# Kernel optimization log

Hardware: AMD Instinct MI355X
Metric: run time of the kernel (lower is better)

## Reference

```python
import jax, jax.numpy as jnp
import numpy as np

B, N, D, C, S = 128, 100000, 256, 2000, 751  # batch, memory size, feat dim, num classes, source classes
TEMP = 0.05
EPS = 1e-06


def _l2norm(x):
    return x / jnp.linalg.norm(x, axis=-1, keepdims=True)


def setup_inputs() -> dict:
    key = jax.random.key(0)
    k1, k2, k3, k4, k5 = jax.random.split(key, 5)
    inputs = _l2norm(jax.random.normal(k1, (B, D), dtype=jnp.float32))
    inputs2 = _l2norm(jax.random.normal(k2, (B, D), dtype=jnp.float32))
    features = _l2norm(jax.random.normal(k3, (N, D), dtype=jnp.float32))
    labels = jax.random.randint(k4, (N,), 0, C)
    labels = labels.at[:C].set(jnp.arange(C))  # ensure labels.max()+1 == C
    indexes = jax.random.randint(k5, (B,), 0, N)
    return {"inputs": inputs, "inputs2": inputs2, "features": features,
            "labels": labels, "indexes": indexes, "source_classes": S}


def reference(inputs, inputs2, features, labels, indexes, source_classes):
    # memory-bank logits, [B, N]
    logits = (inputs @ features.T) / TEMP
    logits2 = (inputs2 @ features.T) / TEMP
    targets = labels[indexes]  # [B]

    # per-class counts and segment-mean of logits over the bank, [C, B]
    nums = jax.ops.segment_sum(jnp.ones((N,), jnp.float32), labels, num_segments=C)  # [C]
    denom = jnp.where(nums > 0, nums, 1.0)[:, None]  # [C, 1]
    sim = jax.ops.segment_sum(logits.T, labels, num_segments=C) / denom   # [C, B]
    sim2 = jax.ops.segment_sum(logits2.T, labels, num_segments=C) / denom  # [C, B]

    # MSE between class-probability maps over the first source_classes classes
    p1 = sim[:source_classes].T   # [B, S]
    p2 = sim2[:source_classes].T  # [B, S]
    diff = jax.nn.softmax(p1, axis=1) - jax.nn.softmax(p2, axis=1)
    loss_mse = jnp.sum(diff * diff) / source_classes

    # hard-positive/negative mining: per-class max of logits (0 for empty classes)
    seg_max = jax.ops.segment_max(logits.T, labels, num_segments=C)  # [C, B], -inf where empty
    present = (nums > 0)  # [C]
    sim_hard = jnp.where(present[:, None], seg_max, 0.0).T  # [B, C]
    # for the target class, use the hardest (min) positive instead
    seg_min = jax.ops.segment_min(logits.T, labels, num_segments=C)  # [C, B]
    b_idx = jnp.arange(B)
    sim_hard = sim_hard.at[b_idx, targets].set(seg_min[targets, b_idx])

    # masked softmax over present classes + NLL
    mask = present.astype(jnp.float32)[None, :]  # [1, C]
    exps = jnp.exp(sim_hard) * mask
    masked_sim = exps / (jnp.sum(exps, axis=1, keepdims=True) + EPS)
    loss_con = -jnp.mean(jnp.log(masked_sim[b_idx, targets] + EPS))

    return (loss_con, loss_mse)
```

## Files before the change

kernel.cpp:

```cpp
#include <hip/hip_runtime.h>
#include <hip/hip_bf16.h>

#define BB 128
#define NN 100000
#define DD 256
#define CC 2000
#define SS 751
#define INVTEMP 20.0f
#define EPSV 1e-6f

#define HIST_BLOCKS 391
#define PREP_BLOCKS 32
#define COPY_BLOCKS 3125
#define NTILES_MAX 3563

typedef __attribute__((ext_vector_type(8))) short bf16x8;
typedef __attribute__((ext_vector_type(8))) unsigned short u16x8;
typedef __attribute__((ext_vector_type(4))) float f32x4;

__device__ __forceinline__ unsigned short f2bf(float x) {
    unsigned int u = __float_as_uint(x);
    u += 0x7fffu + ((u >> 16) & 1u);
    return (unsigned short)(u >> 16);
}

__device__ __forceinline__ u16x8 pack8(float4 a, float4 b) {
    u16x8 o;
    o[0] = f2bf(a.x); o[1] = f2bf(a.y); o[2] = f2bf(a.z); o[3] = f2bf(a.w);
    o[4] = f2bf(b.x); o[5] = f2bf(b.y); o[6] = f2bf(b.z); o[7] = f2bf(b.w);
    return o;
}

__global__ __launch_bounds__(256) void hist_prep_kernel(
    const int* __restrict__ labels, int* __restrict__ counts,
    const float* __restrict__ in1, const float* __restrict__ in2,
    unsigned short* __restrict__ inb)
{
    int bid = blockIdx.x;
    if (bid < HIST_BLOCKS) {
        int n = bid * 256 + threadIdx.x;
        if (n < NN) atomicAdd(&counts[labels[n]], 1);
    } else {
        int ch = (bid - HIST_BLOCKS) * 256 + threadIdx.x;
        if (ch >= 8192) return;
        int l  = ch & 63;
        int kc = (ch >> 6) & 7;
        int nr = ch >> 9;
        int row = nr * 16 + (l & 15);
        const float* src = (row < BB) ? (in1 + (size_t)row * DD)
                                      : (in2 + (size_t)(row - BB) * DD);
        int k0 = kc * 32 + ((l >> 4) << 3);
        u16x8 o;
        #pragma unroll
        for (int j = 0; j < 8; ++j) o[j] = f2bf(src[k0 + j]);
        *(u16x8*)(inb + (size_t)ch * 8) = o;
    }
}

__global__ __launch_bounds__(256) void scan_kernel(const int* __restrict__ counts,
                                                   int* __restrict__ tile_start,
                                                   int* __restrict__ cursor,
                                                   int* __restrict__ tile_meta,
                                                   int* __restrict__ ntiles_total,
                                                   float* __restrict__ out) {
    const int PT = 8;
    int tid = threadIdx.x;
    if (tid == 0) { out[0] = 0.f; out[1] = 0.f; }
    int tcnt[PT];
    int tot = 0;
    #pragma unroll
    for (int i = 0; i < PT; ++i) {
        int c = tid * PT + i;
        tcnt[i] = (c < CC) ? ((counts[c] + 63) >> 6) : 0;
        tot += tcnt[i];
    }
    __shared__ int sh[256];
    sh[tid] = tot;
    __syncthreads();
    for (int ofs = 1; ofs < 256; ofs <<= 1) {
        int v = (tid >= ofs) ? sh[tid - ofs] : 0;
        __syncthreads();
        sh[tid] += v;
        __syncthreads();
    }
    if (tid == 255) *ntiles_total = sh[255];
    int run = sh[tid] - tot;
    #pragma unroll
    for (int i = 0; i < PT; ++i) {
        int c = tid * PT + i;
        if (c < CC) {
            tile_start[c] = run;
            cursor[c] = run << 6;
            for (int j = 0; j < tcnt[i]; ++j)
                tile_meta[run + j] = (c << 5) | j;
        }
        run += tcnt[i];
    }
}

__global__ __launch_bounds__(256) void scatter_conv(
    const int* __restrict__ labels, int* __restrict__ cursor,
    const float* __restrict__ features, unsigned short* __restrict__ featbf)
{
    int t = blockIdx.x * 256 + threadIdx.x;
    int n = t >> 3;
    int g = t & 7;
    int c = labels[n];
    int p = 0;
    if (g == 0) p = atomicAdd(&cursor[c], 1);
    p = __shfl(p, (threadIdx.x & 63) & ~7, 64);

    const float4* src = (const float4*)(features + (size_t)n * DD) + g * 8;
    unsigned short* dst = featbf + (size_t)p * 256 + g * 32;
    #pragma unroll
    for (int i = 0; i < 4; ++i) {
        float4 a = src[2 * i], b = src[2 * i + 1];
        *(u16x8*)(dst + i * 8) = pack8(a, b);
    }
}

__global__ __launch_bounds__(512, 4) void mm_kernel(
    const unsigned short* __restrict__ featbf, const unsigned short* __restrict__ inb,
    const int* __restrict__ tile_meta, const int* __restrict__ counts,
    const int* __restrict__ ntiles_total,
    float* __restrict__ part_max, float* __restrict__ part_min,
    float* __restrict__ part_sA, float* __restrict__ part_sB)
{
    const int t = blockIdx.x;
    if (t >= *ntiles_total) return;
    const int tid = threadIdx.x;
    const int w   = tid >> 6;
    const int l   = tid & 63;
    const int meta = tile_meta[t];
    const int c    = meta >> 5;
    const int base_local = (meta & 31) << 6;
    const int cnt  = counts[c];

    __shared__ __align__(16) char ldsA[32768];

    bf16x8 bfr[16];
    #pragma unroll
    for (int kc = 0; kc < 8; ++kc)
        #pragma unroll
        for (int nb = 0; nb < 2; ++nb) {
            int nr = 2 * w + nb;
            bfr[kc * 2 + nb] = *(const bf16x8*)(inb + (((size_t)(nr * 8 + kc) * 64 + l) << 3));
        }

    const char* Abase = (const char*)featbf + ((size_t)t << 15);
    #pragma unroll
    for (int i = 0; i < 4; ++i) {
        int f   = w * 4 + i;
        int kc  = f & 7;
        int row = ((f >> 3) << 4) + ((l & 15) ^ kc);
        const char* src = Abase + (row << 9) + (kc << 6) + ((l >> 4) << 4);
        __builtin_amdgcn_global_load_lds(
            (const __attribute__((address_space(1))) void*)src,
            (__attribute__((address_space(3))) void*)(&ldsA[0] + (f << 10)),
            16, 0, 0);
    }
    __syncthreads();

    f32x4 acc[4][2];
    #pragma unroll
    for (int ma = 0; ma < 4; ++ma)
        #pragma unroll
        for (int nb = 0; nb < 2; ++nb)
            acc[ma][nb] = (f32x4){0.f, 0.f, 0.f, 0.f};

    __builtin_amdgcn_s_setprio(1);
    #pragma unroll
    for (int kc = 0; kc < 8; ++kc) {
        int lx = (l ^ kc) << 4;
        #pragma unroll
        for (int ma = 0; ma < 4; ++ma) {
            bf16x8 a = *(const bf16x8*)(&ldsA[0] + ((ma * 8 + kc) << 10) + lx);
            acc[ma][0] = __builtin_amdgcn_mfma_f32_16x16x32_bf16(a, bfr[kc * 2 + 0], acc[ma][0], 0, 0, 0);
            acc[ma][1] = __builtin_amdgcn_mfma_f32_16x16x32_bf16(a, bfr[kc * 2 + 1], acc[ma][1], 0, 0, 0);
        }
    }
    __builtin_amdgcn_s_setprio(0);

    const int h4 = (l >> 4) << 2;
    float sm[2] = {0.f, 0.f};
    float mx[2] = {-3.4e38f, -3.4e38f};
    float mn[2] = { 3.4e38f,  3.4e38f};
    #pragma unroll
    for (int ma = 0; ma < 4; ++ma) {
        #pragma unroll
        for (int reg = 0; reg < 4; ++reg) {
            bool valid = (base_local + 16 * ma + h4 + reg) < cnt;
            if (valid) {
                #pragma unroll
                for (int nb = 0; nb < 2; ++nb) {
                    float v = acc[ma][nb][reg];
                    sm[nb] += v;
                    if (w < 4) {
                        mx[nb] = fmaxf(mx[nb], v);
                        mn[nb] = fminf(mn[nb], v);
                    }
                }
            }
        }
    }
    #pragma unroll
    for (int nb = 0; nb < 2; ++nb) {
        sm[nb] += __shfl_xor(sm[nb], 16);
        sm[nb] += __shfl_xor(sm[nb], 32);
        if (w < 4) {
            mx[nb] = fmaxf(mx[nb], __shfl_xor(mx[nb], 16));
            mx[nb] = fmaxf(mx[nb], __shfl_xor(mx[nb], 32));
            mn[nb] = fminf(mn[nb], __shfl_xor(mn[nb], 16));
            mn[nb] = fminf(mn[nb], __shfl_xor(mn[nb], 32));
        }
    }
    if (l < 16) {
        #pragma unroll
        for (int nb = 0; nb < 2; ++nb) {
            int col = 32 * (w & 3) + 16 * nb + l;
            size_t p = (size_t)t * 128 + col;
            if (w < 4) { part_max[p] = mx[nb]; part_min[p] = mn[nb]; part_sA[p] = sm[nb]; }
            else       { part_sB[p] = sm[nb]; }
        }
    }
}

__global__ __launch_bounds__(128) void combine_kernel(
    const float* __restrict__ part_max, const float* __restrict__ part_min,
    const float* __restrict__ part_sA, const float* __restrict__ part_sB,
    const int* __restrict__ tile_start, const int* __restrict__ counts,
    float* __restrict__ gmax, float* __restrict__ gmin,
    float* __restrict__ simA, float* __restrict__ simB)
{
    const int c   = blockIdx.x;
    const int col = threadIdx.x;
    const int cnt = counts[c];
    const size_t o = (size_t)c * 128 + col;
    if (cnt <= 0) {
        gmax[o] = 0.f; gmin[o] = 0.f; simA[o] = 0.f; simB[o] = 0.f;
        return;
    }
    const int t0 = tile_start[c];
    const int nt = (cnt + 63) >> 6;
    float mx = -3.4e38f, mn = 3.4e38f, sA = 0.f, sB = 0.f;
    for (int j = 0; j < nt; ++j) {
        size_t p = (size_t)(t0 + j) * 128 + col;
        mx = fmaxf(mx, part_max[p]);
        mn = fminf(mn, part_min[p]);
        sA += part_sA[p];
        sB += part_sB[p];
    }
    float icnt = INVTEMP / (float)cnt;
    gmax[o] = mx * INVTEMP;
    gmin[o] = mn * INVTEMP;
    simA[o] = sA * icnt;
    simB[o] = sB * icnt;
}


__device__ __forceinline__ float blk_reduce_sum(float v) {
    __shared__ float sh[4];
    int lane = threadIdx.x & 63, w = threadIdx.x >> 6;
    #pragma unroll
    for (int o = 32; o; o >>= 1) v += __shfl_down(v, o, 64);
    __syncthreads();
    if (lane == 0) sh[w] = v;
    __syncthreads();
    return sh[0] + sh[1] + sh[2] + sh[3];
}

__device__ __forceinline__ float blk_reduce_max(float v) {
    __shared__ float sh[4];
    int lane = threadIdx.x & 63, w = threadIdx.x >> 6;
    #pragma unroll
    for (int o = 32; o; o >>= 1) v = fmaxf(v, __shfl_down(v, o, 64));
    __syncthreads();
    if (lane == 0) sh[w] = v;
    __syncthreads();
    return fmaxf(fmaxf(sh[0], sh[1]), fmaxf(sh[2], sh[3]));
}

__global__ __launch_bounds__(256) void finalize_kernel(
    const float* __restrict__ gmax, const float* __restrict__ gmin,
    const float* __restrict__ simA, const float* __restrict__ simB,
    const int* __restrict__ counts, const int* __restrict__ labels,
    const int* __restrict__ indexes, float* __restrict__ out)
{
    const int b   = blockIdx.x;
    const int tid = threadIdx.x;
    const int tgt = labels[indexes[b]];

    __shared__ float sh_etgt;
    float local = 0.f;
    for (int c = tid; c < CC; c += 256) {
        float e = 0.f;
        if (counts[c] > 0) {
            float v = (c == tgt) ? gmin[(size_t)c * 128 + b] : gmax[(size_t)c * 128 + b];
            e = expf(v);
        }
        local += e;
        if (c == tgt) sh_etgt = e;
    }
    float sum_e = blk_reduce_sum(local);
    float etgt = sh_etgt;
    float loss_con_b = -logf(etgt / (sum_e + EPSV) + EPSV);

    __shared__ float a1[SS], a2[SS];
    for (int c = tid; c < SS; c += 256) {
        a1[c] = simA[(size_t)c * 128 + b];
        a2[c] = simB[(size_t)c * 128 + b];
    }
    __syncthreads();
    float m1 = -3.4e38f, m2 = -3.4e38f;
    for (int c = tid; c < SS; c += 256) { m1 = fmaxf(m1, a1[c]); m2 = fmaxf(m2, a2[c]); }
    m1 = blk_reduce_max(m1);
    m2 = blk_reduce_max(m2);
    float s1 = 0.f, s2 = 0.f;
    for (int c = tid; c < SS; c += 256) { s1 += expf(a1[c] - m1); s2 += expf(a2[c] - m2); }
    s1 = blk_reduce_sum(s1);
    s2 = blk_reduce_sum(s2);
    float inv1 = 1.f / s1, inv2 = 1.f / s2;
    float dsum = 0.f;
    for (int c = tid; c < SS; c += 256) {
        float d = expf(a1[c] - m1) * inv1 - expf(a2[c] - m2) * inv2;
        dsum += d * d;
    }
    dsum = blk_reduce_sum(dsum);
    if (tid == 0) {
        atomicAdd(&out[0], loss_con_b * (1.0f / (float)BB));
        atomicAdd(&out[1], dsum * (1.0f / (float)SS));
    }
}


extern "C" void kernel_launch(void* const* d_in, const int* in_sizes, int n_in,
                              void* d_out, int out_size, void* d_ws, size_t ws_size,
                              hipStream_t stream) {
    const float* inputs   = (const float*)d_in[0];
    const float* inputs2  = (const float*)d_in[1];
    const float* features = (const float*)d_in[2];
    const int*   labels   = (const int*)d_in[3];
    const int*   indexes  = (const int*)d_in[4];

    float* out = (float*)d_out;

    int* wsi = (int*)d_ws;
    int* counts     = wsi;
    int* tile_start = wsi + 2048;
    int* cursor     = wsi + 4096;
    int* ntiles     = wsi + 6144;
    unsigned short* inb = (unsigned short*)(wsi + 6160);
    int* tile_meta  = wsi + 38928;
    float* part_max = (float*)(wsi + 42496);
    float* part_min = part_max + (size_t)NTILES_MAX * 128;
    float* part_sA  = part_min + (size_t)NTILES_MAX * 128;
    float* part_sB  = part_sA  + (size_t)NTILES_MAX * 128;
    float* gmax = part_sB + (size_t)NTILES_MAX * 128;
    float* gmin = gmax + (size_t)CC * 128;
    float* simA = gmin + (size_t)CC * 128;
    float* simB = simA + (size_t)CC * 128;
    unsigned short* featbf = (unsigned short*)(simB + (size_t)CC * 128);

    hipMemsetAsync(counts, 0, 2048 * sizeof(int), stream);

    hist_prep_kernel<<<HIST_BLOCKS + PREP_BLOCKS, 256, 0, stream>>>(
        labels, counts, inputs, inputs2, inb);
    scan_kernel<<<1, 256, 0, stream>>>(counts, tile_start, cursor, tile_meta, ntiles, out);
    scatter_conv<<<COPY_BLOCKS, 256, 0, stream>>>(labels, cursor, features, featbf);
    mm_kernel<<<NTILES_MAX, 512, 0, stream>>>(featbf, inb, tile_meta, counts, ntiles,
                                              part_max, part_min, part_sA, part_sB);
    combine_kernel<<<CC, 128, 0, stream>>>(part_max, part_min, part_sA, part_sB,
                                           tile_start, counts, gmax, gmin, simA, simB);
    finalize_kernel<<<BB, 256, 0, stream>>>(gmax, gmin, simA, simB, counts,
                                            labels, indexes, out);
}
```

Before: 103.4 us.

## Process two tiles per matmul block and fold combine into finalize

The matmul kernel now loads two feature tiles into a doubled LDS buffer per block, reusing the register-resident input fragments across both tiles and halving the block count. The separate per-class combine kernel is removed, and finalize reads tile partials directly, computing class max/min/mean per batch column. This saves one launch and the intermediate global arrays. In exchange, LDS use per block doubles, which may reduce occupancy, and finalize does strided partial reads with only 128 blocks.

```diff
diff --git a/kernel.cpp b/kernel.cpp
--- a/kernel.cpp
+++ b/kernel.cpp
@@ -13,6 +13,7 @@
 #define PREP_BLOCKS 32
 #define COPY_BLOCKS 3125
 #define NTILES_MAX 3563
+#define NBLK2 1782
 
 typedef __attribute__((ext_vector_type(8))) short bf16x8;
 typedef __attribute__((ext_vector_type(8))) unsigned short u16x8;
@@ -126,17 +127,14 @@
     float* __restrict__ part_max, float* __restrict__ part_min,
     float* __restrict__ part_sA, float* __restrict__ part_sB)
 {
-    const int t = blockIdx.x;
-    if (t >= *ntiles_total) return;
+    const int ntt = *ntiles_total;
+    const int t0g = 2 * blockIdx.x;
+    if (t0g >= ntt) return;
     const int tid = threadIdx.x;
     const int w   = tid >> 6;
     const int l   = tid & 63;
-    const int meta = tile_meta[t];
-    const int c    = meta >> 5;
-    const int base_local = (meta & 31) << 6;
-    const int cnt  = counts[c];
-
-    __shared__ __align__(16) char ldsA[32768];
+
+    __shared__ __align__(16) char ldsA[2][32768];
 
     bf16x8 bfr[16];
     #pragma unroll
@@ -147,170 +145,170 @@
             bfr[kc * 2 + nb] = *(const bf16x8*)(inb + (((size_t)(nr * 8 + kc) * 64 + l) << 3));
         }
 
-    const char* Abase = (const char*)featbf + ((size_t)t << 15);
-    #pragma unroll
-    for (int i = 0; i < 4; ++i) {
-        int f   = w * 4 + i;
-        int kc  = f & 7;
-        int row = ((f >> 3) << 4) + ((l & 15) ^ kc);
-        const char* src = Abase + (row << 9) + (kc << 6) + ((l >> 4) << 4);
-        __builtin_amdgcn_global_load_lds(
-            (const __attribute__((address_space(1))) void*)src,
-            (__attribute__((address_space(3))) void*)(&ldsA[0] + (f << 10)),
-            16, 0, 0);
-    }
-    __syncthreads();
-
-    f32x4 acc[4][2];
-    #pragma unroll
-    for (int ma = 0; ma < 4; ++ma)
-        #pragma unroll
-        for (int nb = 0; nb < 2; ++nb)
-            acc[ma][nb] = (f32x4){0.f, 0.f, 0.f, 0.f};
-
-    __builtin_amdgcn_s_setprio(1);
-    #pragma unroll
-    for (int kc = 0; kc < 8; ++kc) {
-        int lx = (l ^ kc) << 4;
+    const int ntiles_here = min(2, ntt - t0g);
+    for (int tt = 0; tt < ntiles_here; ++tt) {
+        const char* Abase = (const char*)featbf + ((size_t)(t0g + tt) << 15);
+        #pragma unroll
+        for (int i = 0; i < 4; ++i) {
+            int f   = w * 4 + i;
+            int kc  = f & 7;
+            int row = ((f >> 3) << 4) + ((l & 15) ^ kc);
+            const char* src = Abase + (row << 9) + (kc << 6) + ((l >> 4) << 4);
+            __builtin_amdgcn_global_load_lds(
+                (const __attribute__((address_space(1))) void*)src,
+                (__attribute__((address_space(3))) void*)(&ldsA[tt][0] + (f << 10)),
+                16, 0, 0);
+        }
+    }
+    __syncthreads();
+
+    const int h4 = (l >> 4) << 2;
+    for (int tt = 0; tt < ntiles_here; ++tt) {
+        const int t    = t0g + tt;
+        const int meta = tile_meta[t];
+        const int c    = meta >> 5;
+        const int base_local = (meta & 31) << 6;
+        const int cnt  = counts[c];
+        const char* L  = &ldsA[tt][0];
+
+        f32x4 acc[4][2];
+        #pragma unroll
+        for (int ma = 0; ma < 4; ++ma)
+            #pragma unroll
+            for (int nb = 0; nb < 2; ++nb)
+                acc[ma][nb] = (f32x4){0.f, 0.f, 0.f, 0.f};
+
+        __builtin_amdgcn_s_setprio(1);
+        #pragma unroll
+        for (int kc = 0; kc < 8; ++kc) {
+            int lx = (l ^ kc) << 4;
+            #pragma unroll
+            for (int ma = 0; ma < 4; ++ma) {
+                bf16x8 a = *(const bf16x8*)(L + ((ma * 8 + kc) << 10) + lx);
+                acc[ma][0] = __builtin_amdgcn_mfma_f32_16x16x32_bf16(a, bfr[kc * 2 + 0], acc[ma][0], 0, 0, 0);
+                acc[ma][1] = __builtin_amdgcn_mfma_f32_16x16x32_bf16(a, bfr[kc * 2 + 1], acc[ma][1], 0, 0, 0);
+            }
+        }
+        __builtin_amdgcn_s_setprio(0);
+
+        float sm[2] = {0.f, 0.f};
+        float mx[2] = {-3.4e38f, -3.4e38f};
+        float mn[2] = { 3.4e38f,  3.4e38f};
         #pragma unroll
         for (int ma = 0; ma < 4; ++ma) {
-            bf16x8 a = *(const bf16x8*)(&ldsA[0] + ((ma * 8 + kc) << 10) + lx);
-            acc[ma][0] = __builtin_amdgcn_mfma_f32_16x16x32_bf16(a, bfr[kc * 2 + 0], acc[ma][0], 0, 0, 0);
-            acc[ma][1] = __builtin_amdgcn_mfma_f32_16x16x32_bf16(a, bfr[kc * 2 + 1], acc[ma][1], 0, 0, 0);
-        }
-    }
-    __builtin_amdgcn_s_setprio(0);
-
-    const int h4 = (l >> 4) << 2;
-    float sm[2] = {0.f, 0.f};
-    float mx[2] = {-3.4e38f, -3.4e38f};
-    float mn[2] = { 3.4e38f,  3.4e38f};
-    #pragma unroll
-    for (int ma = 0; ma < 4; ++ma) {
-        #pragma unroll
-        for (int reg = 0; reg < 4; ++reg) {
-            bool valid = (base_local + 16 * ma + h4 + reg) < cnt;
-            if (valid) {
-                #pragma unroll
-                for (int nb = 0; nb < 2; ++nb) {
-                    float v = acc[ma][nb][reg];
-                    sm[nb] += v;
-                    if (w < 4) {
-                        mx[nb] = fmaxf(mx[nb], v);
-                        mn[nb] = fminf(mn[nb], v);
+            #pragma unroll
+            for (int reg = 0; reg < 4; ++reg) {
+                bool valid = (base_local + 16 * ma + h4 + reg) < cnt;
+                if (valid) {
+                    #pragma unroll
+                    for (int nb = 0; nb < 2; ++nb) {
+                        float v = acc[ma][nb][reg];
+                        sm[nb] += v;
+                        if (w < 4) {
+                            mx[nb] = fmaxf(mx[nb], v);
+                            mn[nb] = fminf(mn[nb], v);
+                        }
                     }
                 }
             }
         }
-    }
-    #pragma unroll
-    for (int nb = 0; nb < 2; ++nb) {
-        sm[nb] += __shfl_xor(sm[nb], 16);
-        sm[nb] += __shfl_xor(sm[nb], 32);
-        if (w < 4) {
-            mx[nb] = fmaxf(mx[nb], __shfl_xor(mx[nb], 16));
-            mx[nb] = fmaxf(mx[nb], __shfl_xor(mx[nb], 32));
-            mn[nb] = fminf(mn[nb], __shfl_xor(mn[nb], 16));
-            mn[nb] = fminf(mn[nb], __shfl_xor(mn[nb], 32));
-        }
-    }
-    if (l < 16) {
         #pragma unroll
         for (int nb = 0; nb < 2; ++nb) {
-            int col = 32 * (w & 3) + 16 * nb + l;
-            size_t p = (size_t)t * 128 + col;
-            if (w < 4) { part_max[p] = mx[nb]; part_min[p] = mn[nb]; part_sA[p] = sm[nb]; }
-            else       { part_sB[p] = sm[nb]; }
-        }
-    }
-}
-
-__global__ __launch_bounds__(128) void combine_kernel(
+            sm[nb] += __shfl_xor(sm[nb], 16);
+            sm[nb] += __shfl_xor(sm[nb], 32);
+            if (w < 4) {
+                mx[nb] = fmaxf(mx[nb], __shfl_xor(mx[nb], 16));
+                mx[nb] = fmaxf(mx[nb], __shfl_xor(mx[nb], 32));
+                mn[nb] = fminf(mn[nb], __shfl_xor(mn[nb], 16));
+                mn[nb] = fminf(mn[nb], __shfl_xor(mn[nb], 32));
+            }
+        }
+        if (l < 16) {
+            #pragma unroll
+            for (int nb = 0; nb < 2; ++nb) {
+                int col = 32 * (w & 3) + 16 * nb + l;
+                size_t p = (size_t)t * 128 + col;
+                if (w < 4) { part_max[p] = mx[nb]; part_min[p] = mn[nb]; part_sA[p] = sm[nb]; }
+                else       { part_sB[p] = sm[nb]; }
+            }
+        }
+    }
+}
+
+
+__device__ __forceinline__ float blk_reduce_sum(float v) {
+    __shared__ float sh[4];
+    int lane = threadIdx.x & 63, w = threadIdx.x >> 6;
+    #pragma unroll
+    for (int o = 32; o; o >>= 1) v += __shfl_down(v, o, 64);
+    __syncthreads();
+    if (lane == 0) sh[w] = v;
+    __syncthreads();
+    return sh[0] + sh[1] + sh[2] + sh[3];
+}
+
+__device__ __forceinline__ float blk_reduce_max(float v) {
+    __shared__ float sh[4];
+    int lane = threadIdx.x & 63, w = threadIdx.x >> 6;
+    #pragma unroll
+    for (int o = 32; o; o >>= 1) v = fmaxf(v, __shfl_down(v, o, 64));
+    __syncthreads();
+    if (lane == 0) sh[w] = v;
+    __syncthreads();
+    return fmaxf(fmaxf(sh[0], sh[1]), fmaxf(sh[2], sh[3]));
+}
+
+__global__ __launch_bounds__(256) void finalize_kernel(
     const float* __restrict__ part_max, const float* __restrict__ part_min,
     const float* __restrict__ part_sA, const float* __restrict__ part_sB,
     const int* __restrict__ tile_start, const int* __restrict__ counts,
-    float* __restrict__ gmax, float* __restrict__ gmin,
-    float* __restrict__ simA, float* __restrict__ simB)
-{
-    const int c   = blockIdx.x;
-    const int col = threadIdx.x;
-    const int cnt = counts[c];
-    const size_t o = (size_t)c * 128 + col;
-    if (cnt <= 0) {
-        gmax[o] = 0.f; gmin[o] = 0.f; simA[o] = 0.f; simB[o] = 0.f;
-        return;
-    }
-    const int t0 = tile_start[c];
-    const int nt = (cnt + 63) >> 6;
-    float mx = -3.4e38f, mn = 3.4e38f, sA = 0.f, sB = 0.f;
-    for (int j = 0; j < nt; ++j) {
-        size_t p = (size_t)(t0 + j) * 128 + col;
-        mx = fmaxf(mx, part_max[p]);
-        mn = fminf(mn, part_min[p]);
-        sA += part_sA[p];
-        sB += part_sB[p];
-    }
-    float icnt = INVTEMP / (float)cnt;
-    gmax[o] = mx * INVTEMP;
-    gmin[o] = mn * INVTEMP;
-    simA[o] = sA * icnt;
-    simB[o] = sB * icnt;
-}
-
-
-__device__ __forceinline__ float blk_reduce_sum(float v) {
-    __shared__ float sh[4];
-    int lane = threadIdx.x & 63, w = threadIdx.x >> 6;
-    #pragma unroll
-    for (int o = 32; o; o >>= 1) v += __shfl_down(v, o, 64);
-    __syncthreads();
-    if (lane == 0) sh[w] = v;
-    __syncthreads();
-    return sh[0] + sh[1] + sh[2] + sh[3];
-}
-
-__device__ __forceinline__ float blk_reduce_max(float v) {
-    __shared__ float sh[4];
-    int lane = threadIdx.x & 63, w = threadIdx.x >> 6;
-    #pragma unroll
-    for (int o = 32; o; o >>= 1) v = fmaxf(v, __shfl_down(v, o, 64));
-    __syncthreads();
-    if (lane == 0) sh[w] = v;
-    __syncthreads();
-    return fmaxf(fmaxf(sh[0], sh[1]), fmaxf(sh[2], sh[3]));
-}
-
-__global__ __launch_bounds__(256) void finalize_kernel(
-    const float* __restrict__ gmax, const float* __restrict__ gmin,
-    const float* __restrict__ simA, const float* __restrict__ simB,
-    const int* __restrict__ counts, const int* __restrict__ labels,
-    const int* __restrict__ indexes, float* __restrict__ out)
+    const int* __restrict__ labels, const int* __restrict__ indexes,
+    float* __restrict__ out)
 {
     const int b   = blockIdx.x;
     const int tid = threadIdx.x;
     const int tgt = labels[indexes[b]];
 
+    __shared__ float a1[SS], a2[SS];
     __shared__ float sh_etgt;
+
     float local = 0.f;
     for (int c = tid; c < CC; c += 256) {
-        float e = 0.f;
-        if (counts[c] > 0) {
-            float v = (c == tgt) ? gmin[(size_t)c * 128 + b] : gmax[(size_t)c * 128 + b];
-            e = expf(v);
-        }
-        local += e;
-        if (c == tgt) sh_etgt = e;
+        int cnt = counts[c];
+        if (cnt > 0) {
+            int t0 = tile_start[c];
+            int nt = (cnt + 63) >> 6;
+            bool src = (c < SS);
+            float mx = -3.4e38f, sA = 0.f, sB = 0.f;
+            for (int j = 0; j < nt; ++j) {
+                size_t p = (size_t)(t0 + j) * 128 + b;
+                mx = fmaxf(mx, part_max[p]);
+                if (src) { sA += part_sA[p]; sB += part_sB[p]; }
+            }
+            float v = mx;
+            if (c == tgt) {
+                float mn = 3.4e38f;
+                for (int j = 0; j < nt; ++j)
+                    mn = fminf(mn, part_min[(size_t)(t0 + j) * 128 + b]);
+                v = mn;
+            }
+            float e = expf(v * INVTEMP);
+            local += e;
+            if (c == tgt) sh_etgt = e;
+            if (src) {
+                float icnt = INVTEMP / (float)cnt;
+                a1[c] = sA * icnt;
+                a2[c] = sB * icnt;
+            }
+        } else if (c < SS) {
+            a1[c] = 0.f;
+            a2[c] = 0.f;
+        }
     }
     float sum_e = blk_reduce_sum(local);
     float etgt = sh_etgt;
     float loss_con_b = -logf(etgt / (sum_e + EPSV) + EPSV);
 
-    __shared__ float a1[SS], a2[SS];
-    for (int c = tid; c < SS; c += 256) {
-        a1[c] = simA[(size_t)c * 128 + b];
-        a2[c] = simB[(size_t)c * 128 + b];
-    }
-    __syncthreads();
     float m1 = -3.4e38f, m2 = -3.4e38f;
     for (int c = tid; c < SS; c += 256) { m1 = fmaxf(m1, a1[c]); m2 = fmaxf(m2, a2[c]); }
     m1 = blk_reduce_max(m1);
@@ -355,11 +353,7 @@
     float* part_min = part_max + (size_t)NTILES_MAX * 128;
     float* part_sA  = part_min + (size_t)NTILES_MAX * 128;
     float* part_sB  = part_sA  + (size_t)NTILES_MAX * 128;
-    float* gmax = part_sB + (size_t)NTILES_MAX * 128;
-    float* gmin = gmax + (size_t)CC * 128;
-    float* simA = gmin + (size_t)CC * 128;
-    float* simB = simA + (size_t)CC * 128;
-    unsigned short* featbf = (unsigned short*)(simB + (size_t)CC * 128);
+    unsigned short* featbf = (unsigned short*)(part_sB + (size_t)NTILES_MAX * 128);
 
     hipMemsetAsync(counts, 0, 2048 * sizeof(int), stream);
 
@@ -367,10 +361,8 @@
         labels, counts, inputs, inputs2, inb);
     scan_kernel<<<1, 256, 0, stream>>>(counts, tile_start, cursor, tile_meta, ntiles, out);
     scatter_conv<<<COPY_BLOCKS, 256, 0, stream>>>(labels, cursor, features, featbf);
-    mm_kernel<<<NTILES_MAX, 512, 0, stream>>>(featbf, inb, tile_meta, counts, ntiles,
-                                              part_max, part_min, part_sA, part_sB);
-    combine_kernel<<<CC, 128, 0, stream>>>(part_max, part_min, part_sA, part_sB,
-                                           tile_start, counts, gmax, gmin, simA, simB);
-    finalize_kernel<<<BB, 256, 0, stream>>>(gmax, gmin, simA, simB, counts,
-                                            labels, indexes, out);
-}
+    mm_kernel<<<NBLK2, 512, 0, stream>>>(featbf, inb, tile_meta, counts, ntiles,
+                                         part_max, part_min, part_sA, part_sB);
+    finalize_kernel<<<BB, 256, 0, stream>>>(part_max, part_min, part_sA, part_sB,
+                                            tile_start, counts, labels, indexes, out);
+}
```

Result: slower. 107.8 us (+4.3%).
